# Performance work log

Measured on AMD Instinct MI355X. Metric: run time of the kernel, lower is better.

Reference implementation:

```python
import jax, jax.numpy as jnp
import numpy as np

R = 8192            # reservoir_size
CORE = int(R * 0.6)          # 4915
SHELL = int(R * 0.3)         # 2457
FB = R - CORE - SHELL        # 820
H = 1024            # lstm_hidden
IN = 1              # input_size
OUT = 1             # output_size
LEAK = 0.1
SPECTRAL = 0.9
SPARSITY = 0.3


def _scaled(key, n):
    # uniform(-1,1) NxN; spectral radius of such a matrix ~ sqrt(n * var) = sqrt(n/3).
    # Scale to ~SPECTRAL (mimics the SVD-based scaling at init without the O(n^3) SVD).
    W = jax.random.uniform(key, (n, n), jnp.float32, -1.0, 1.0)
    return W * (SPECTRAL / jnp.sqrt(n / 3.0))


def setup_inputs() -> dict:
    key = jax.random.key(0)
    ks = jax.random.split(key, 20)
    u = lambda k, sh: jax.random.uniform(k, sh, jnp.float32, -1.0, 1.0)

    W_in = u(ks[0], (R, IN))
    W_core = _scaled(ks[1], CORE)
    mask_shell = (jax.random.uniform(ks[2], (SHELL, SHELL)) < SPARSITY).astype(jnp.float32)
    W_shell = _scaled(ks[3], SHELL) * mask_shell
    W_feedback = _scaled(ks[4], FB)
    W_shell_core = u(ks[5], (CORE, SHELL))
    W_feedback_core = u(ks[6], (CORE, FB))
    dopamine = jnp.float32(0.5)
    omega = jnp.ones((R,), jnp.float32) * 2.0
    gamma = jnp.ones((R,), jnp.float32) * 0.1

    # PyTorch LSTM params, gate order [i, f, g, o]
    s = 1.0 / np.sqrt(H)
    W_ih = jax.random.uniform(ks[7], (4 * H, R), jnp.float32, -s, s)
    W_hh = jax.random.uniform(ks[8], (4 * H, H), jnp.float32, -s, s)
    b_ih = jax.random.uniform(ks[9], (4 * H,), jnp.float32, -s, s)
    b_hh = jax.random.uniform(ks[10], (4 * H,), jnp.float32, -s, s)

    W_out = jax.random.uniform(ks[11], (OUT, H), jnp.float32, -s, s)
    b_out = jax.random.uniform(ks[12], (OUT,), jnp.float32, -s, s)

    x = jax.random.normal(ks[13], (IN,), jnp.float32)
    state = jax.random.normal(ks[14], (1, R), jnp.float32)
    lstm_hidden = jax.random.normal(ks[15], (1, 1, H), jnp.float32)
    lstm_cell = jax.random.normal(ks[16], (1, 1, H), jnp.float32)

    return dict(x=x, state=state, lstm_hidden=lstm_hidden, lstm_cell=lstm_cell,
                W_in=W_in, W_core=W_core, W_shell=W_shell, W_feedback=W_feedback,
                W_shell_core=W_shell_core, W_feedback_core=W_feedback_core,
                dopamine=dopamine, omega=omega, gamma=gamma,
                W_ih=W_ih, W_hh=W_hh, b_ih=b_ih, b_hh=b_hh,
                W_out=W_out, b_out=b_out)


def reference(x, state, lstm_hidden, lstm_cell,
              W_in, W_core, W_shell, W_feedback, W_shell_core, W_feedback_core,
              dopamine, omega, gamma, W_ih, W_hh, b_ih, b_hh, W_out, b_out):
    reservoir_in = W_in @ x                      # (R,)
    core = state[:, :CORE]                       # (1, CORE)
    shell = state[:, CORE:CORE + SHELL]          # (1, SHELL)
    fb = state[:, -FB:]                          # (1, FB)

    core_pred = jnp.tanh(core @ W_core.T + reservoir_in[:CORE][None, :])
    shell_pred = jnp.tanh(shell @ W_shell.T)
    fb_pred = jnp.tanh(fb @ W_feedback.T)
    core_pred = core_pred + jnp.tanh(shell_pred @ W_shell_core.T) \
                          + jnp.tanh(fb_pred @ W_feedback_core.T)

    core_new = (1.0 - LEAK) * core + LEAK * core_pred
    shell_new = (1.0 - LEAK) * shell + LEAK * shell_pred
    fb_new = (1.0 - LEAK) * fb + LEAK * fb_pred
    s = jnp.concatenate([core_new, shell_new, fb_new], axis=1)  # (1, R)

    # harmonic oscillator update + dopamine scaling
    s = s + 0.1 * (omega * s - gamma * jnp.tanh(s))
    s = dopamine * s

    # single LSTM cell step (torch gate order i, f, g, o)
    h = lstm_hidden[0]  # (1, H)
    c = lstm_cell[0]    # (1, H)
    gates = s @ W_ih.T + b_ih + h @ W_hh.T + b_hh   # (1, 4H)
    i, f, g, o = jnp.split(gates, 4, axis=1)
    c_new = jax.nn.sigmoid(f) * c + jax.nn.sigmoid(i) * jnp.tanh(g)
    h_new = jax.nn.sigmoid(o) * jnp.tanh(c_new)

    output = h_new @ W_out.T + b_out             # (1, OUT)
    return output, s, h_new[None], c_new[None]
```

## Files before the change

kernel.cpp:

```cpp
#include <hip/hip_runtime.h>
#include <math.h>

#define R_TOT 8192
#define CORE  4915
#define SHELL 2457
#define FB    820
#define H     1024

__device__ __align__(16) float g_pred1[R_TOT];
__device__ __align__(16) float g_s[R_TOT];
__device__ __align__(16) float g_gates[4 * H];

__device__ __forceinline__ int swz(int i) { return i + (i >> 5); }
#define SWZ_SIZE(n) ((n) + (((n) - 1) >> 5))

__device__ __forceinline__ float waveReduce(float v) {
  #pragma unroll
  for (int off = 32; off; off >>= 1) v += __shfl_down(v, off, 64);
  return v;
}

__device__ __forceinline__ float sigm(float x) { return 1.f / (1.f + expf(-x)); }
__device__ __forceinline__ float dot4(float4 a, float4 b) {
  return a.x * b.x + a.y * b.y + a.z * b.z + a.w * b.w;
}

__device__ __forceinline__ float dotRowSw(const float* __restrict__ w,
                                          const float* __restrict__ xs,
                                          int xb, int N, int lane) {
  uintptr_t a = (uintptr_t)w;
  int head = (int)(((16 - (a & 15)) & 15) >> 2);
  if (head > N) head = N;
  float s0 = 0.f, s1 = 0.f, s2 = 0.f, s3 = 0.f,
        s4 = 0.f, s5 = 0.f, s6 = 0.f, s7 = 0.f;
  if (lane < head) s0 += w[lane] * xs[swz(xb + lane)];
  int nC = (N - head) >> 2;
  const float4* wv = (const float4*)(w + head);
  int b0 = xb + head;
  int c = lane;
  for (; c + 448 < nC; c += 512) {
    float4 v0 = wv[c],       v1 = wv[c + 64],  v2 = wv[c + 128], v3 = wv[c + 192],
           v4 = wv[c + 256], v5 = wv[c + 320], v6 = wv[c + 384], v7 = wv[c + 448];
    int i0 = b0 + (c << 2);
    s0 += v0.x*xs[swz(i0     )] + v0.y*xs[swz(i0+   1)] + v0.z*xs[swz(i0+   2)] + v0.w*xs[swz(i0+   3)];
    s1 += v1.x*xs[swz(i0+ 256)] + v1.y*xs[swz(i0+ 257)] + v1.z*xs[swz(i0+ 258)] + v1.w*xs[swz(i0+ 259)];
    s2 += v2.x*xs[swz(i0+ 512)] + v2.y*xs[swz(i0+ 513)] + v2.z*xs[swz(i0+ 514)] + v2.w*xs[swz(i0+ 515)];
    s3 += v3.x*xs[swz(i0+ 768)] + v3.y*xs[swz(i0+ 769)] + v3.z*xs[swz(i0+ 770)] + v3.w*xs[swz(i0+ 771)];
    s4 += v4.x*xs[swz(i0+1024)] + v4.y*xs[swz(i0+1025)] + v4.z*xs[swz(i0+1026)] + v4.w*xs[swz(i0+1027)];
    s5 += v5.x*xs[swz(i0+1280)] + v5.y*xs[swz(i0+1281)] + v5.z*xs[swz(i0+1282)] + v5.w*xs[swz(i0+1283)];
    s6 += v6.x*xs[swz(i0+1536)] + v6.y*xs[swz(i0+1537)] + v6.z*xs[swz(i0+1538)] + v6.w*xs[swz(i0+1539)];
    s7 += v7.x*xs[swz(i0+1792)] + v7.y*xs[swz(i0+1793)] + v7.z*xs[swz(i0+1794)] + v7.w*xs[swz(i0+1795)];
  }
  for (; c + 192 < nC; c += 256) {
    float4 v0 = wv[c], v1 = wv[c + 64], v2 = wv[c + 128], v3 = wv[c + 192];
    int i0 = b0 + (c << 2);
    s0 += v0.x*xs[swz(i0    )] + v0.y*xs[swz(i0+  1)] + v0.z*xs[swz(i0+  2)] + v0.w*xs[swz(i0+  3)];
    s1 += v1.x*xs[swz(i0+256)] + v1.y*xs[swz(i0+257)] + v1.z*xs[swz(i0+258)] + v1.w*xs[swz(i0+259)];
    s2 += v2.x*xs[swz(i0+512)] + v2.y*xs[swz(i0+513)] + v2.z*xs[swz(i0+514)] + v2.w*xs[swz(i0+515)];
    s3 += v3.x*xs[swz(i0+768)] + v3.y*xs[swz(i0+769)] + v3.z*xs[swz(i0+770)] + v3.w*xs[swz(i0+771)];
  }
  for (; c < nC; c += 64) {
    float4 v = wv[c];
    int i0 = b0 + (c << 2);
    s1 += v.x*xs[swz(i0)] + v.y*xs[swz(i0+1)] + v.z*xs[swz(i0+2)] + v.w*xs[swz(i0+3)];
  }
  for (int i = head + (nC << 2) + lane; i < N; i += 64)
    s2 += w[i] * xs[swz(xb + i)];
  return ((s0 + s1) + (s2 + s3)) + ((s4 + s5) + (s6 + s7));
}

__device__ __forceinline__ float dotRowAl(const float4* __restrict__ wv,
                                          const float4* __restrict__ xs4,
                                          int nC, int lane) {
  float s0 = 0.f, s1 = 0.f, s2 = 0.f, s3 = 0.f,
        s4 = 0.f, s5 = 0.f, s6 = 0.f, s7 = 0.f;
  int c = lane;
  for (; c + 448 < nC; c += 512) {
    float4 v0 = wv[c],       v1 = wv[c + 64],  v2 = wv[c + 128], v3 = wv[c + 192],
           v4 = wv[c + 256], v5 = wv[c + 320], v6 = wv[c + 384], v7 = wv[c + 448];
    s0 += dot4(v0, xs4[c      ]); s1 += dot4(v1, xs4[c + 64 ]);
    s2 += dot4(v2, xs4[c + 128]); s3 += dot4(v3, xs4[c + 192]);
    s4 += dot4(v4, xs4[c + 256]); s5 += dot4(v5, xs4[c + 320]);
    s6 += dot4(v6, xs4[c + 384]); s7 += dot4(v7, xs4[c + 448]);
  }
  for (; c + 192 < nC; c += 256) {
    float4 v0 = wv[c], v1 = wv[c + 64], v2 = wv[c + 128], v3 = wv[c + 192];
    s0 += dot4(v0, xs4[c      ]); s1 += dot4(v1, xs4[c + 64 ]);
    s2 += dot4(v2, xs4[c + 128]); s3 += dot4(v3, xs4[c + 192]);
  }
  for (; c < nC; c += 64) s1 += dot4(wv[c], xs4[c]);
  return ((s0 + s1) + (s2 + s3)) + ((s4 + s5) + (s6 + s7));
}

__device__ __forceinline__ void s_update(int i, float pred,
                                         const float* __restrict__ state,
                                         const float* __restrict__ omega,
                                         const float* __restrict__ gamma,
                                         float dopa, float* __restrict__ dout) {
  float old = state[i];
  float s1 = 0.9f * old + 0.1f * pred;
  float s2 = s1 + 0.1f * (omega[i] * s1 - gamma[i] * tanhf(s1));
  float s3 = dopa * s2;
  g_s[i] = s3;
  dout[1 + i] = s3;
}

#define NB1_CORE  ((CORE  + 3) / 4)
#define NB1_SHELL ((SHELL + 3) / 4)
#define NB1_WHH   (4 * H / 4)
#define NB1_FB    ((FB    + 3) / 4)
#define NB1_TOT   (NB1_CORE + NB1_SHELL + NB1_WHH + NB1_FB)

__global__ __launch_bounds__(256, 4) void k_stage1(
    const float* __restrict__ state, const float* __restrict__ Wcore,
    const float* __restrict__ Wshell, const float* __restrict__ Wfb,
    const float* __restrict__ Win, const float* __restrict__ xin,
    const float* __restrict__ Whh, const float* __restrict__ hin) {
  __shared__ __align__(16) float xs[SWZ_SIZE(CORE)];
  int b = blockIdx.x;
  int tid = threadIdx.x, wave = tid >> 6, lane = tid & 63;
  if (b < NB1_CORE) {
    for (int i = tid; i < CORE; i += 256) xs[swz(i)] = state[i];
    __syncthreads();
    int r = b * 4 + wave;
    if (r >= CORE) return;
    float sum = waveReduce(dotRowSw(Wcore + (size_t)r * CORE, xs, 0, CORE, lane));
    if (lane == 0) g_pred1[r] = tanhf(sum + Win[r] * xin[0]);
  } else if (b < NB1_CORE + NB1_SHELL) {
    for (int i = tid; i < SHELL; i += 256) xs[swz(i)] = state[CORE + i];
    __syncthreads();
    int r = (b - NB1_CORE) * 4 + wave;
    if (r >= SHELL) return;
    float sum = waveReduce(dotRowSw(Wshell + (size_t)r * SHELL, xs, 0, SHELL, lane));
    if (lane == 0) g_pred1[CORE + r] = tanhf(sum);
  } else if (b < NB1_CORE + NB1_SHELL + NB1_WHH) {
    float4* xs4 = (float4*)xs;
    const float4* h4 = (const float4*)hin;
    for (int i = tid; i < H / 4; i += 256) xs4[i] = h4[i];
    __syncthreads();
    int r = (b - NB1_CORE - NB1_SHELL) * 4 + wave;
    float sum = waveReduce(dotRowAl((const float4*)(Whh + (size_t)r * H), xs4, H / 4, lane));
    if (lane == 0) g_gates[r] = sum;
  } else {
    float4* xs4 = (float4*)xs;
    const float4* f4 = (const float4*)(state + CORE + SHELL);
    for (int i = tid; i < FB / 4; i += 256) xs4[i] = f4[i];
    __syncthreads();
    int r = (b - NB1_CORE - NB1_SHELL - NB1_WHH) * 4 + wave;
    if (r >= FB) return;
    float sum = waveReduce(dotRowAl((const float4*)(Wfb + (size_t)r * FB), xs4, FB / 4, lane));
    if (lane == 0) g_pred1[CORE + SHELL + r] = tanhf(sum);
  }
}

#define NB2_CORE ((CORE + 3) / 4)
#define NB2_EW   ((SHELL + FB + 255) / 256)

__global__ __launch_bounds__(256, 4) void k_stage2(
    const float* __restrict__ state,
    const float* __restrict__ Wsc, const float* __restrict__ Wfc,
    const float* __restrict__ omega, const float* __restrict__ gamma,
    const float* __restrict__ dopamine, float* __restrict__ dout) {
  __shared__ __align__(16) float  xsS[SWZ_SIZE(SHELL)];
  __shared__ __align__(16) float4 xsF[FB / 4];
  float dopa = dopamine[0];
  int b = blockIdx.x, tid = threadIdx.x;
  if (b < NB2_CORE) {
    for (int i = tid; i < SHELL; i += 256) xsS[swz(i)] = g_pred1[CORE + i];
    const float4* f4 = (const float4*)(g_pred1 + CORE + SHELL);
    for (int i = tid; i < FB / 4; i += 256) xsF[i] = f4[i];
    __syncthreads();
    int wave = tid >> 6, lane = tid & 63;
    int r = b * 4 + wave;
    if (r >= CORE) return;
    float d1 = waveReduce(dotRowSw(Wsc + (size_t)r * SHELL, xsS, 0, SHELL, lane));
    float d2 = waveReduce(dotRowAl((const float4*)(Wfc + (size_t)r * FB), xsF, FB / 4, lane));
    if (lane == 0) {
      float pred = g_pred1[r] + tanhf(d1) + tanhf(d2);
      s_update(r, pred, state, omega, gamma, dopa, dout);
    }
  } else {
    int i = CORE + (b - NB2_CORE) * 256 + tid;
    if (i < R_TOT) s_update(i, g_pred1[i], state, omega, gamma, dopa, dout);
  }
}

__global__ __launch_bounds__(256, 4) void k_gates(
    const float* __restrict__ Wih,
    const float* __restrict__ bih, const float* __restrict__ bhh) {
  __shared__ __align__(16) float4 xs4[R_TOT / 4];
  int tid = threadIdx.x;
  const float4* s4 = (const float4*)g_s;
  for (int i = tid; i < R_TOT / 4; i += 256) xs4[i] = s4[i];
  __syncthreads();
  int wave = tid >> 6, lane = tid & 63;
  int r = blockIdx.x * 4 + wave;
  float sum = waveReduce(dotRowAl((const float4*)(Wih + (size_t)r * R_TOT), xs4, R_TOT / 4, lane));
  if (lane == 0) g_gates[r] += sum + bih[r] + bhh[r];
}

__global__ __launch_bounds__(1024) void k_lstm(
    const float* __restrict__ c_in, const float* __restrict__ Wout,
    const float* __restrict__ bout, float* __restrict__ dout) {
  __shared__ float red[16];
  int j = threadIdx.x;
  float ig = g_gates[j], fg = g_gates[H + j], gg = g_gates[2 * H + j], og = g_gates[3 * H + j];
  float c = c_in[j];
  float cn = sigm(fg) * c + sigm(ig) * tanhf(gg);
  float hn = sigm(og) * tanhf(cn);
  dout[1 + R_TOT + j] = hn;
  dout[1 + R_TOT + H + j] = cn;
  float w = Wout[j] * hn;
  w = waveReduce(w);
  int wave = j >> 6, lane = j & 63;
  if (lane == 0) red[wave] = w;
  __syncthreads();
  if (j == 0) {
    float t = 0.f;
    #pragma unroll
    for (int k = 0; k < 16; ++k) t += red[k];
    dout[0] = t + bout[0];
  }
}

extern "C" void kernel_launch(void* const* d_in, const int* in_sizes, int n_in,
                              void* d_out, int out_size, void* d_ws, size_t ws_size,
                              hipStream_t stream) {
  const float *x = 0, *state = 0, *h = 0, *c = 0, *Win = 0, *Wcore = 0, *Wshell = 0,
              *Wfb = 0, *Wsc = 0, *Wfc = 0, *dopa = 0, *omega = 0, *gamma = 0,
              *Wih = 0, *Whh = 0, *bih = 0, *bhh = 0, *Wout = 0, *bout = 0;
  int n1 = 0, n1024 = 0, n8192 = 0, n4096 = 0;
  for (int i = 0; i < n_in; ++i) {
    const float* p = (const float*)d_in[i];
    switch (in_sizes[i]) {
      case 24157225: Wcore = p; break;
      case 6036849:  Wshell = p; break;
      case 672400:   Wfb = p; break;
      case 12076155: Wsc = p; break;
      case 4030300:  Wfc = p; break;
      case 33554432: Wih = p; break;
      case 4194304:  Whh = p; break;
      case 1:    { if (n1 == 0) x = p; else if (n1 == 1) dopa = p; else bout = p; n1++; } break;
      case 1024: { if (n1024 == 0) h = p; else if (n1024 == 1) c = p; else Wout = p; n1024++; } break;
      case 8192: { if (n8192 == 0) state = p; else if (n8192 == 1) Win = p;
                   else if (n8192 == 2) omega = p; else gamma = p; n8192++; } break;
      case 4096: { if (n4096 == 0) bih = p; else bhh = p; n4096++; } break;
      default: break;
    }
  }
  float* dout = (float*)d_out;

  k_stage1<<<NB1_TOT, 256, 0, stream>>>(state, Wcore, Wshell, Wfb, Win, x, Whh, h);
  k_stage2<<<NB2_CORE + NB2_EW, 256, 0, stream>>>(state, Wsc, Wfc, omega, gamma, dopa, dout);
  k_gates<<<(4 * H) / 4, 256, 0, stream>>>(Wih, bih, bhh);
  k_lstm<<<1, 1024, 0, stream>>>(c, Wout, bout, dout);
}
```

Baseline: 367.0 us.

## Compute two rows per wave and fold LSTM step into gates kernel

```diff
diff --git a/kernel.cpp b/kernel.cpp
--- a/kernel.cpp
+++ b/kernel.cpp
@@ -10,6 +10,7 @@
 __device__ __align__(16) float g_pred1[R_TOT];
 __device__ __align__(16) float g_s[R_TOT];
 __device__ __align__(16) float g_gates[4 * H];
+__device__ int g_done = 0;
 
 __device__ __forceinline__ int swz(int i) { return i + (i >> 5); }
 #define SWZ_SIZE(n) ((n) + (((n) - 1) >> 5))
@@ -25,35 +26,106 @@
   return a.x * b.x + a.y * b.y + a.z * b.z + a.w * b.w;
 }
 
+__device__ __forceinline__ float2 dotRow2Sw(const float* __restrict__ wA,
+                                            const float* __restrict__ wB,
+                                            const float* __restrict__ xs,
+                                            int N, int lane) {
+  uintptr_t a = (uintptr_t)wA;
+  int head = (int)(((16 - (a & 15)) & 15) >> 2);
+  if (head > N) head = N;
+  float a0 = 0.f, a1 = 0.f, a2 = 0.f, a3 = 0.f;
+  float b0 = 0.f, b1 = 0.f, b2 = 0.f, b3 = 0.f;
+  if (lane < head) {
+    float xv = xs[swz(lane)];
+    a0 += wA[lane] * xv; b0 += wB[lane] * xv;
+  }
+  int nC = (N - head) >> 2;
+  const float4* va = (const float4*)(wA + head);
+  const float4* vb = (const float4*)(wB + head);
+  int c = lane;
+  #define CH2(Ak, Bk, off, accA, accB) { int ii = i0 + (off);                 \
+      float x0_ = xs[swz(ii)],     x1_ = xs[swz(ii + 1)],                     \
+            x2_ = xs[swz(ii + 2)], x3_ = xs[swz(ii + 3)];                     \
+      accA += Ak.x * x0_ + Ak.y * x1_ + Ak.z * x2_ + Ak.w * x3_;              \
+      accB += Bk.x * x0_ + Bk.y * x1_ + Bk.z * x2_ + Bk.w * x3_; }
+  for (; c + 448 < nC; c += 512) {
+    float4 A0 = va[c],       A1 = va[c + 64],  A2 = va[c + 128], A3 = va[c + 192],
+           A4 = va[c + 256], A5 = va[c + 320], A6 = va[c + 384], A7 = va[c + 448];
+    float4 B0 = vb[c],       B1 = vb[c + 64],  B2 = vb[c + 128], B3 = vb[c + 192],
+           B4 = vb[c + 256], B5 = vb[c + 320], B6 = vb[c + 384], B7 = vb[c + 448];
+    int i0 = head + (c << 2);
+    CH2(A0, B0, 0,    a0, b0) CH2(A1, B1, 256,  a1, b1)
+    CH2(A2, B2, 512,  a2, b2) CH2(A3, B3, 768,  a3, b3)
+    CH2(A4, B4, 1024, a0, b0) CH2(A5, B5, 1280, a1, b1)
+    CH2(A6, B6, 1536, a2, b2) CH2(A7, B7, 1792, a3, b3)
+  }
+  for (; c + 192 < nC; c += 256) {
+    float4 A0 = va[c], A1 = va[c + 64], A2 = va[c + 128], A3 = va[c + 192];
+    float4 B0 = vb[c], B1 = vb[c + 64], B2 = vb[c + 128], B3 = vb[c + 192];
+    int i0 = head + (c << 2);
+    CH2(A0, B0, 0,   a0, b0) CH2(A1, B1, 256, a1, b1)
+    CH2(A2, B2, 512, a2, b2) CH2(A3, B3, 768, a3, b3)
+  }
+  for (; c < nC; c += 64) {
+    float4 A0 = va[c], B0 = vb[c];
+    int i0 = head + (c << 2);
+    CH2(A0, B0, 0, a0, b0)
+  }
+  #undef CH2
+  for (int i = head + (nC << 2) + lane; i < N; i += 64) {
+    float xv = xs[swz(i)];
+    a2 += wA[i] * xv; b2 += wB[i] * xv;
+  }
+  return make_float2((a0 + a1) + (a2 + a3), (b0 + b1) + (b2 + b3));
+}
+
+__device__ __forceinline__ float2 dotRow2Al(const float4* __restrict__ wa,
+                                            const float4* __restrict__ wb,
+                                            const float4* __restrict__ xs4,
+                                            int nC, int lane) {
+  float a0 = 0.f, a1 = 0.f, a2 = 0.f, a3 = 0.f;
+  float b0 = 0.f, b1 = 0.f, b2 = 0.f, b3 = 0.f;
+  int c = lane;
+  for (; c + 448 < nC; c += 512) {
+    float4 A0 = wa[c],       A1 = wa[c + 64],  A2 = wa[c + 128], A3 = wa[c + 192],
+           A4 = wa[c + 256], A5 = wa[c + 320], A6 = wa[c + 384], A7 = wa[c + 448];
+    float4 B0 = wb[c],       B1 = wb[c + 64],  B2 = wb[c + 128], B3 = wb[c + 192],
+           B4 = wb[c + 256], B5 = wb[c + 320], B6 = wb[c + 384], B7 = wb[c + 448];
+    float4 X0 = xs4[c],       X1 = xs4[c + 64],  X2 = xs4[c + 128], X3 = xs4[c + 192],
+           X4 = xs4[c + 256], X5 = xs4[c + 320], X6 = xs4[c + 384], X7 = xs4[c + 448];
+    a0 += dot4(A0, X0); b0 += dot4(B0, X0); a1 += dot4(A1, X1); b1 += dot4(B1, X1);
+    a2 += dot4(A2, X2); b2 += dot4(B2, X2); a3 += dot4(A3, X3); b3 += dot4(B3, X3);
+    a0 += dot4(A4, X4); b0 += dot4(B4, X4); a1 += dot4(A5, X5); b1 += dot4(B5, X5);
+    a2 += dot4(A6, X6); b2 += dot4(B6, X6); a3 += dot4(A7, X7); b3 += dot4(B7, X7);
+  }
+  for (; c + 192 < nC; c += 256) {
+    float4 A0 = wa[c], A1 = wa[c + 64], A2 = wa[c + 128], A3 = wa[c + 192];
+    float4 B0 = wb[c], B1 = wb[c + 64], B2 = wb[c + 128], B3 = wb[c + 192];
+    float4 X0 = xs4[c], X1 = xs4[c + 64], X2 = xs4[c + 128], X3 = xs4[c + 192];
+    a0 += dot4(A0, X0); b0 += dot4(B0, X0); a1 += dot4(A1, X1); b1 += dot4(B1, X1);
+    a2 += dot4(A2, X2); b2 += dot4(B2, X2); a3 += dot4(A3, X3); b3 += dot4(B3, X3);
+  }
+  for (; c < nC; c += 64) {
+    float4 A0 = wa[c], B0 = wb[c], X0 = xs4[c];
+    a0 += dot4(A0, X0); b0 += dot4(B0, X0);
+  }
+  return make_float2((a0 + a1) + (a2 + a3), (b0 + b1) + (b2 + b3));
+}
+
 __device__ __forceinline__ float dotRowSw(const float* __restrict__ w,
                                           const float* __restrict__ xs,
-                                          int xb, int N, int lane) {
+                                          int N, int lane) {
   uintptr_t a = (uintptr_t)w;
   int head = (int)(((16 - (a & 15)) & 15) >> 2);
   if (head > N) head = N;
-  float s0 = 0.f, s1 = 0.f, s2 = 0.f, s3 = 0.f,
-        s4 = 0.f, s5 = 0.f, s6 = 0.f, s7 = 0.f;
-  if (lane < head) s0 += w[lane] * xs[swz(xb + lane)];
+  float s0 = 0.f, s1 = 0.f, s2 = 0.f, s3 = 0.f;
+  if (lane < head) s0 += w[lane] * xs[swz(lane)];
   int nC = (N - head) >> 2;
   const float4* wv = (const float4*)(w + head);
-  int b0 = xb + head;
   int c = lane;
-  for (; c + 448 < nC; c += 512) {
-    float4 v0 = wv[c],       v1 = wv[c + 64],  v2 = wv[c + 128], v3 = wv[c + 192],
-           v4 = wv[c + 256], v5 = wv[c + 320], v6 = wv[c + 384], v7 = wv[c + 448];
-    int i0 = b0 + (c << 2);
-    s0 += v0.x*xs[swz(i0     )] + v0.y*xs[swz(i0+   1)] + v0.z*xs[swz(i0+   2)] + v0.w*xs[swz(i0+   3)];
-    s1 += v1.x*xs[swz(i0+ 256)] + v1.y*xs[swz(i0+ 257)] + v1.z*xs[swz(i0+ 258)] + v1.w*xs[swz(i0+ 259)];
-    s2 += v2.x*xs[swz(i0+ 512)] + v2.y*xs[swz(i0+ 513)] + v2.z*xs[swz(i0+ 514)] + v2.w*xs[swz(i0+ 515)];
-    s3 += v3.x*xs[swz(i0+ 768)] + v3.y*xs[swz(i0+ 769)] + v3.z*xs[swz(i0+ 770)] + v3.w*xs[swz(i0+ 771)];
-    s4 += v4.x*xs[swz(i0+1024)] + v4.y*xs[swz(i0+1025)] + v4.z*xs[swz(i0+1026)] + v4.w*xs[swz(i0+1027)];
-    s5 += v5.x*xs[swz(i0+1280)] + v5.y*xs[swz(i0+1281)] + v5.z*xs[swz(i0+1282)] + v5.w*xs[swz(i0+1283)];
-    s6 += v6.x*xs[swz(i0+1536)] + v6.y*xs[swz(i0+1537)] + v6.z*xs[swz(i0+1538)] + v6.w*xs[swz(i0+1539)];
-    s7 += v7.x*xs[swz(i0+1792)] + v7.y*xs[swz(i0+1793)] + v7.z*xs[swz(i0+1794)] + v7.w*xs[swz(i0+1795)];
-  }
   for (; c + 192 < nC; c += 256) {
     float4 v0 = wv[c], v1 = wv[c + 64], v2 = wv[c + 128], v3 = wv[c + 192];
-    int i0 = b0 + (c << 2);
+    int i0 = head + (c << 2);
     s0 += v0.x*xs[swz(i0    )] + v0.y*xs[swz(i0+  1)] + v0.z*xs[swz(i0+  2)] + v0.w*xs[swz(i0+  3)];
     s1 += v1.x*xs[swz(i0+256)] + v1.y*xs[swz(i0+257)] + v1.z*xs[swz(i0+258)] + v1.w*xs[swz(i0+259)];
     s2 += v2.x*xs[swz(i0+512)] + v2.y*xs[swz(i0+513)] + v2.z*xs[swz(i0+514)] + v2.w*xs[swz(i0+515)];
@@ -61,35 +133,26 @@
   }
   for (; c < nC; c += 64) {
     float4 v = wv[c];
-    int i0 = b0 + (c << 2);
+    int i0 = head + (c << 2);
     s1 += v.x*xs[swz(i0)] + v.y*xs[swz(i0+1)] + v.z*xs[swz(i0+2)] + v.w*xs[swz(i0+3)];
   }
   for (int i = head + (nC << 2) + lane; i < N; i += 64)
-    s2 += w[i] * xs[swz(xb + i)];
-  return ((s0 + s1) + (s2 + s3)) + ((s4 + s5) + (s6 + s7));
+    s2 += w[i] * xs[swz(i)];
+  return (s0 + s1) + (s2 + s3);
 }
 
 __device__ __forceinline__ float dotRowAl(const float4* __restrict__ wv,
                                           const float4* __restrict__ xs4,
                                           int nC, int lane) {
-  float s0 = 0.f, s1 = 0.f, s2 = 0.f, s3 = 0.f,
-        s4 = 0.f, s5 = 0.f, s6 = 0.f, s7 = 0.f;
+  float s0 = 0.f, s1 = 0.f, s2 = 0.f, s3 = 0.f;
   int c = lane;
-  for (; c + 448 < nC; c += 512) {
-    float4 v0 = wv[c],       v1 = wv[c + 64],  v2 = wv[c + 128], v3 = wv[c + 192],
-           v4 = wv[c + 256], v5 = wv[c + 320], v6 = wv[c + 384], v7 = wv[c + 448];
-    s0 += dot4(v0, xs4[c      ]); s1 += dot4(v1, xs4[c + 64 ]);
-    s2 += dot4(v2, xs4[c + 128]); s3 += dot4(v3, xs4[c + 192]);
-    s4 += dot4(v4, xs4[c + 256]); s5 += dot4(v5, xs4[c + 320]);
-    s6 += dot4(v6, xs4[c + 384]); s7 += dot4(v7, xs4[c + 448]);
-  }
   for (; c + 192 < nC; c += 256) {
     float4 v0 = wv[c], v1 = wv[c + 64], v2 = wv[c + 128], v3 = wv[c + 192];
-    s0 += dot4(v0, xs4[c      ]); s1 += dot4(v1, xs4[c + 64 ]);
+    s0 += dot4(v0, xs4[c]);       s1 += dot4(v1, xs4[c + 64]);
     s2 += dot4(v2, xs4[c + 128]); s3 += dot4(v3, xs4[c + 192]);
   }
-  for (; c < nC; c += 64) s1 += dot4(wv[c], xs4[c]);
-  return ((s0 + s1) + (s2 + s3)) + ((s4 + s5) + (s6 + s7));
+  for (; c < nC; c += 64) s0 += dot4(wv[c], xs4[c]);
+  return (s0 + s1) + (s2 + s3);
 }
 
 __device__ __forceinline__ void s_update(int i, float pred,
@@ -105,11 +168,11 @@
   dout[1 + i] = s3;
 }
 
-#define NB1_CORE  ((CORE  + 3) / 4)
-#define NB1_SHELL ((SHELL + 3) / 4)
-#define NB1_WHH   (4 * H / 4)
-#define NB1_FB    ((FB    + 3) / 4)
-#define NB1_TOT   (NB1_CORE + NB1_SHELL + NB1_WHH + NB1_FB)
+#define NB1_CORE8  ((CORE + 7) / 8)
+#define NB1_SHELL8 ((SHELL + 7) / 8)
+#define NB1_WHH8   (4 * H / 8)
+#define NB1_FB8    ((FB + 7) / 8)
+#define NB1_TOT    (NB1_CORE8 + NB1_SHELL8 + NB1_WHH8 + NB1_FB8)
 
 __global__ __launch_bounds__(256, 4) void k_stage1(
     const float* __restrict__ state, const float* __restrict__ Wcore,
@@ -117,44 +180,77 @@
     const float* __restrict__ Win, const float* __restrict__ xin,
     const float* __restrict__ Whh, const float* __restrict__ hin) {
   __shared__ __align__(16) float xs[SWZ_SIZE(CORE)];
-  int b = blockIdx.x;
-  int tid = threadIdx.x, wave = tid >> 6, lane = tid & 63;
-  if (b < NB1_CORE) {
+  int b = blockIdx.x, tid = threadIdx.x, wave = tid >> 6, lane = tid & 63;
+  if (b < NB1_CORE8) {
     for (int i = tid; i < CORE; i += 256) xs[swz(i)] = state[i];
     __syncthreads();
-    int r = b * 4 + wave;
-    if (r >= CORE) return;
-    float sum = waveReduce(dotRowSw(Wcore + (size_t)r * CORE, xs, 0, CORE, lane));
-    if (lane == 0) g_pred1[r] = tanhf(sum + Win[r] * xin[0]);
-  } else if (b < NB1_CORE + NB1_SHELL) {
+    int rA = b * 8 + wave, rB = rA + 4;
+    if (rA >= CORE) return;
+    float x0 = xin[0];
+    if (rB < CORE) {
+      float2 d = dotRow2Sw(Wcore + (size_t)rA * CORE, Wcore + (size_t)rB * CORE,
+                           xs, CORE, lane);
+      d.x = waveReduce(d.x); d.y = waveReduce(d.y);
+      if (lane == 0) {
+        g_pred1[rA] = tanhf(d.x + Win[rA] * x0);
+        g_pred1[rB] = tanhf(d.y + Win[rB] * x0);
+      }
+    } else {
+      float s = waveReduce(dotRowSw(Wcore + (size_t)rA * CORE, xs, CORE, lane));
+      if (lane == 0) g_pred1[rA] = tanhf(s + Win[rA] * x0);
+    }
+  } else if (b < NB1_CORE8 + NB1_SHELL8) {
     for (int i = tid; i < SHELL; i += 256) xs[swz(i)] = state[CORE + i];
     __syncthreads();
-    int r = (b - NB1_CORE) * 4 + wave;
-    if (r >= SHELL) return;
-    float sum = waveReduce(dotRowSw(Wshell + (size_t)r * SHELL, xs, 0, SHELL, lane));
-    if (lane == 0) g_pred1[CORE + r] = tanhf(sum);
-  } else if (b < NB1_CORE + NB1_SHELL + NB1_WHH) {
+    int rA = (b - NB1_CORE8) * 8 + wave, rB = rA + 4;
+    if (rA >= SHELL) return;
+    if (rB < SHELL) {
+      float2 d = dotRow2Sw(Wshell + (size_t)rA * SHELL, Wshell + (size_t)rB * SHELL,
+                           xs, SHELL, lane);
+      d.x = waveReduce(d.x); d.y = waveReduce(d.y);
+      if (lane == 0) {
+        g_pred1[CORE + rA] = tanhf(d.x);
+        g_pred1[CORE + rB] = tanhf(d.y);
+      }
+    } else {
+      float s = waveReduce(dotRowSw(Wshell + (size_t)rA * SHELL, xs, SHELL, lane));
+      if (lane == 0) g_pred1[CORE + rA] = tanhf(s);
+    }
+  } else if (b < NB1_CORE8 + NB1_SHELL8 + NB1_WHH8) {
     float4* xs4 = (float4*)xs;
     const float4* h4 = (const float4*)hin;
     for (int i = tid; i < H / 4; i += 256) xs4[i] = h4[i];
     __syncthreads();
-    int r = (b - NB1_CORE - NB1_SHELL) * 4 + wave;
-    float sum = waveReduce(dotRowAl((const float4*)(Whh + (size_t)r * H), xs4, H / 4, lane));
-    if (lane == 0) g_gates[r] = sum;
+    int rA = (b - NB1_CORE8 - NB1_SHELL8) * 8 + wave, rB = rA + 4;
+    float2 d = dotRow2Al((const float4*)(Whh + (size_t)rA * H),
+                         (const float4*)(Whh + (size_t)rB * H), xs4, H / 4, lane);
+    d.x = waveReduce(d.x); d.y = waveReduce(d.y);
+    if (lane == 0) { g_gates[rA] = d.x; g_gates[rB] = d.y; }
   } else {
     float4* xs4 = (float4*)xs;
     const float4* f4 = (const float4*)(state + CORE + SHELL);
     for (int i = tid; i < FB / 4; i += 256) xs4[i] = f4[i];
     __syncthreads();
-    int r = (b - NB1_CORE - NB1_SHELL - NB1_WHH) * 4 + wave;
-    if (r >= FB) return;
-    float sum = waveReduce(dotRowAl((const float4*)(Wfb + (size_t)r * FB), xs4, FB / 4, lane));
-    if (lane == 0) g_pred1[CORE + SHELL + r] = tanhf(sum);
-  }
-}
-
-#define NB2_CORE ((CORE + 3) / 4)
-#define NB2_EW   ((SHELL + FB + 255) / 256)
+    int rA = (b - NB1_CORE8 - NB1_SHELL8 - NB1_WHH8) * 8 + wave, rB = rA + 4;
+    if (rA >= FB) return;
+    if (rB < FB) {
+      float2 d = dotRow2Al((const float4*)(Wfb + (size_t)rA * FB),
+                           (const float4*)(Wfb + (size_t)rB * FB), xs4, FB / 4, lane);
+      d.x = waveReduce(d.x); d.y = waveReduce(d.y);
+      if (lane == 0) {
+        g_pred1[CORE + SHELL + rA] = tanhf(d.x);
+        g_pred1[CORE + SHELL + rB] = tanhf(d.y);
+      }
+    } else {
+      float s = waveReduce(dotRowAl((const float4*)(Wfb + (size_t)rA * FB),
+                                    xs4, FB / 4, lane));
+      if (lane == 0) g_pred1[CORE + SHELL + rA] = tanhf(s);
+    }
+  }
+}
+
+#define NB2_CORE8 ((CORE + 7) / 8)
+#define NB2_EW    ((SHELL + FB + 255) / 256)
 
 __global__ __launch_bounds__(256, 4) void k_stage2(
     const float* __restrict__ state,
@@ -165,62 +261,86 @@
   __shared__ __align__(16) float4 xsF[FB / 4];
   float dopa = dopamine[0];
   int b = blockIdx.x, tid = threadIdx.x;
-  if (b < NB2_CORE) {
+  if (b < NB2_CORE8) {
     for (int i = tid; i < SHELL; i += 256) xsS[swz(i)] = g_pred1[CORE + i];
     const float4* f4 = (const float4*)(g_pred1 + CORE + SHELL);
     for (int i = tid; i < FB / 4; i += 256) xsF[i] = f4[i];
     __syncthreads();
     int wave = tid >> 6, lane = tid & 63;
-    int r = b * 4 + wave;
-    if (r >= CORE) return;
-    float d1 = waveReduce(dotRowSw(Wsc + (size_t)r * SHELL, xsS, 0, SHELL, lane));
-    float d2 = waveReduce(dotRowAl((const float4*)(Wfc + (size_t)r * FB), xsF, FB / 4, lane));
-    if (lane == 0) {
-      float pred = g_pred1[r] + tanhf(d1) + tanhf(d2);
-      s_update(r, pred, state, omega, gamma, dopa, dout);
+    int rA = b * 8 + wave, rB = rA + 4;
+    if (rA >= CORE) return;
+    if (rB < CORE) {
+      float2 d1 = dotRow2Sw(Wsc + (size_t)rA * SHELL, Wsc + (size_t)rB * SHELL,
+                            xsS, SHELL, lane);
+      float2 d2 = dotRow2Al((const float4*)(Wfc + (size_t)rA * FB),
+                            (const float4*)(Wfc + (size_t)rB * FB), xsF, FB / 4, lane);
+      d1.x = waveReduce(d1.x); d1.y = waveReduce(d1.y);
+      d2.x = waveReduce(d2.x); d2.y = waveReduce(d2.y);
+      if (lane == 0) {
+        s_update(rA, g_pred1[rA] + tanhf(d1.x) + tanhf(d2.x), state, omega, gamma, dopa, dout);
+        s_update(rB, g_pred1[rB] + tanhf(d1.y) + tanhf(d2.y), state, omega, gamma, dopa, dout);
+      }
+    } else {
+      float d1 = waveReduce(dotRowSw(Wsc + (size_t)rA * SHELL, xsS, SHELL, lane));
+      float d2 = waveReduce(dotRowAl((const float4*)(Wfc + (size_t)rA * FB),
+                                     xsF, FB / 4, lane));
+      if (lane == 0)
+        s_update(rA, g_pred1[rA] + tanhf(d1) + tanhf(d2), state, omega, gamma, dopa, dout);
     }
   } else {
-    int i = CORE + (b - NB2_CORE) * 256 + tid;
+    int i = CORE + (b - NB2_CORE8) * 256 + tid;
     if (i < R_TOT) s_update(i, g_pred1[i], state, omega, gamma, dopa, dout);
   }
 }
+
+#define NBG (4 * H / 8)
 
 __global__ __launch_bounds__(256, 4) void k_gates(
     const float* __restrict__ Wih,
-    const float* __restrict__ bih, const float* __restrict__ bhh) {
+    const float* __restrict__ bih, const float* __restrict__ bhh,
+    const float* __restrict__ cin, const float* __restrict__ Wout,
+    const float* __restrict__ bout, float* __restrict__ dout) {
   __shared__ __align__(16) float4 xs4[R_TOT / 4];
-  int tid = threadIdx.x;
+  __shared__ float red[4];
+  __shared__ int s_last;
+  int tid = threadIdx.x, wave = tid >> 6, lane = tid & 63;
   const float4* s4 = (const float4*)g_s;
   for (int i = tid; i < R_TOT / 4; i += 256) xs4[i] = s4[i];
   __syncthreads();
-  int wave = tid >> 6, lane = tid & 63;
-  int r = blockIdx.x * 4 + wave;
-  float sum = waveReduce(dotRowAl((const float4*)(Wih + (size_t)r * R_TOT), xs4, R_TOT / 4, lane));
-  if (lane == 0) g_gates[r] += sum + bih[r] + bhh[r];
-}
-
-__global__ __launch_bounds__(1024) void k_lstm(
-    const float* __restrict__ c_in, const float* __restrict__ Wout,
-    const float* __restrict__ bout, float* __restrict__ dout) {
-  __shared__ float red[16];
-  int j = threadIdx.x;
-  float ig = g_gates[j], fg = g_gates[H + j], gg = g_gates[2 * H + j], og = g_gates[3 * H + j];
-  float c = c_in[j];
-  float cn = sigm(fg) * c + sigm(ig) * tanhf(gg);
-  float hn = sigm(og) * tanhf(cn);
-  dout[1 + R_TOT + j] = hn;
-  dout[1 + R_TOT + H + j] = cn;
-  float w = Wout[j] * hn;
-  w = waveReduce(w);
-  int wave = j >> 6, lane = j & 63;
-  if (lane == 0) red[wave] = w;
+  int rA = blockIdx.x * 8 + wave, rB = rA + 4;
+  float2 d = dotRow2Al((const float4*)(Wih + (size_t)rA * R_TOT),
+                       (const float4*)(Wih + (size_t)rB * R_TOT),
+                       xs4, R_TOT / 4, lane);
+  d.x = waveReduce(d.x); d.y = waveReduce(d.y);
+  if (lane == 0) {
+    g_gates[rA] += d.x + bih[rA] + bhh[rA];
+    g_gates[rB] += d.y + bih[rB] + bhh[rB];
+  }
+  __threadfence();
   __syncthreads();
-  if (j == 0) {
-    float t = 0.f;
-    #pragma unroll
-    for (int k = 0; k < 16; ++k) t += red[k];
-    dout[0] = t + bout[0];
-  }
+  if (tid == 0) {
+    int prev = atomicAdd(&g_done, 1);
+    s_last = (prev == (int)gridDim.x - 1);
+    if (s_last) atomicExch(&g_done, 0);
+  }
+  __syncthreads();
+  if (!s_last) return;
+  __threadfence();
+  float acc = 0.f;
+  for (int j = tid; j < H; j += 256) {
+    float ig = g_gates[j], fg = g_gates[H + j];
+    float gg = g_gates[2 * H + j], og = g_gates[3 * H + j];
+    float cc = cin[j];
+    float cn = sigm(fg) * cc + sigm(ig) * tanhf(gg);
+    float hn = sigm(og) * tanhf(cn);
+    dout[1 + R_TOT + j] = hn;
+    dout[1 + R_TOT + H + j] = cn;
+    acc += Wout[j] * hn;
+  }
+  acc = waveReduce(acc);
+  if (lane == 0) red[wave] = acc;
+  __syncthreads();
+  if (tid == 0) dout[0] = red[0] + red[1] + red[2] + red[3] + bout[0];
 }
 
 extern "C" void kernel_launch(void* const* d_in, const int* in_sizes, int n_in,
@@ -251,7 +371,6 @@
   float* dout = (float*)d_out;
 
   k_stage1<<<NB1_TOT, 256, 0, stream>>>(state, Wcore, Wshell, Wfb, Win, x, Whh, h);
-  k_stage2<<<NB2_CORE + NB2_EW, 256, 0, stream>>>(state, Wsc, Wfc, omega, gamma, dopa, dout);
-  k_gates<<<(4 * H) / 4, 256, 0, stream>>>(Wih, bih, bhh);
-  k_lstm<<<1, 1024, 0, stream>>>(c, Wout, bout, dout);
-}
+  k_stage2<<<NB2_CORE8 + NB2_EW, 256, 0, stream>>>(state, Wsc, Wfc, omega, gamma, dopa, dout);
+  k_gates<<<NBG, 256, 0, stream>>>(Wih, bih, bhh, c, Wout, bout, dout);
+}
```

New measurement: 428.0 us. 16.6% more time.

## Split W_ih gate GEMV across K-chunks and drop shared-memory swizzle

Applied to the files above, without the earlier changes.

```diff
diff --git a/kernel.cpp b/kernel.cpp
--- a/kernel.cpp
+++ b/kernel.cpp
@@ -10,9 +10,7 @@
 __device__ __align__(16) float g_pred1[R_TOT];
 __device__ __align__(16) float g_s[R_TOT];
 __device__ __align__(16) float g_gates[4 * H];
-
-__device__ __forceinline__ int swz(int i) { return i + (i >> 5); }
-#define SWZ_SIZE(n) ((n) + (((n) - 1) >> 5))
+__device__ __align__(16) float g_gpart[4][4 * H];
 
 __device__ __forceinline__ float waveReduce(float v) {
   #pragma unroll
@@ -27,69 +25,66 @@
 
 __device__ __forceinline__ float dotRowSw(const float* __restrict__ w,
                                           const float* __restrict__ xs,
-                                          int xb, int N, int lane) {
+                                          int N, int lane) {
   uintptr_t a = (uintptr_t)w;
   int head = (int)(((16 - (a & 15)) & 15) >> 2);
   if (head > N) head = N;
-  float s0 = 0.f, s1 = 0.f, s2 = 0.f, s3 = 0.f,
-        s4 = 0.f, s5 = 0.f, s6 = 0.f, s7 = 0.f;
-  if (lane < head) s0 += w[lane] * xs[swz(xb + lane)];
+  float s0 = 0.f, s1 = 0.f, s2 = 0.f, s3 = 0.f;
+  if (lane < head) s0 += w[lane] * xs[lane];
   int nC = (N - head) >> 2;
   const float4* wv = (const float4*)(w + head);
-  int b0 = xb + head;
   int c = lane;
   for (; c + 448 < nC; c += 512) {
     float4 v0 = wv[c],       v1 = wv[c + 64],  v2 = wv[c + 128], v3 = wv[c + 192],
            v4 = wv[c + 256], v5 = wv[c + 320], v6 = wv[c + 384], v7 = wv[c + 448];
-    int i0 = b0 + (c << 2);
-    s0 += v0.x*xs[swz(i0     )] + v0.y*xs[swz(i0+   1)] + v0.z*xs[swz(i0+   2)] + v0.w*xs[swz(i0+   3)];
-    s1 += v1.x*xs[swz(i0+ 256)] + v1.y*xs[swz(i0+ 257)] + v1.z*xs[swz(i0+ 258)] + v1.w*xs[swz(i0+ 259)];
-    s2 += v2.x*xs[swz(i0+ 512)] + v2.y*xs[swz(i0+ 513)] + v2.z*xs[swz(i0+ 514)] + v2.w*xs[swz(i0+ 515)];
-    s3 += v3.x*xs[swz(i0+ 768)] + v3.y*xs[swz(i0+ 769)] + v3.z*xs[swz(i0+ 770)] + v3.w*xs[swz(i0+ 771)];
-    s4 += v4.x*xs[swz(i0+1024)] + v4.y*xs[swz(i0+1025)] + v4.z*xs[swz(i0+1026)] + v4.w*xs[swz(i0+1027)];
-    s5 += v5.x*xs[swz(i0+1280)] + v5.y*xs[swz(i0+1281)] + v5.z*xs[swz(i0+1282)] + v5.w*xs[swz(i0+1283)];
-    s6 += v6.x*xs[swz(i0+1536)] + v6.y*xs[swz(i0+1537)] + v6.z*xs[swz(i0+1538)] + v6.w*xs[swz(i0+1539)];
-    s7 += v7.x*xs[swz(i0+1792)] + v7.y*xs[swz(i0+1793)] + v7.z*xs[swz(i0+1794)] + v7.w*xs[swz(i0+1795)];
+    int i0 = head + (c << 2);
+    s0 += v0.x*xs[i0     ] + v0.y*xs[i0+   1] + v0.z*xs[i0+   2] + v0.w*xs[i0+   3];
+    s1 += v1.x*xs[i0+ 256] + v1.y*xs[i0+ 257] + v1.z*xs[i0+ 258] + v1.w*xs[i0+ 259];
+    s2 += v2.x*xs[i0+ 512] + v2.y*xs[i0+ 513] + v2.z*xs[i0+ 514] + v2.w*xs[i0+ 515];
+    s3 += v3.x*xs[i0+ 768] + v3.y*xs[i0+ 769] + v3.z*xs[i0+ 770] + v3.w*xs[i0+ 771];
+    s0 += v4.x*xs[i0+1024] + v4.y*xs[i0+1025] + v4.z*xs[i0+1026] + v4.w*xs[i0+1027];
+    s1 += v5.x*xs[i0+1280] + v5.y*xs[i0+1281] + v5.z*xs[i0+1282] + v5.w*xs[i0+1283];
+    s2 += v6.x*xs[i0+1536] + v6.y*xs[i0+1537] + v6.z*xs[i0+1538] + v6.w*xs[i0+1539];
+    s3 += v7.x*xs[i0+1792] + v7.y*xs[i0+1793] + v7.z*xs[i0+1794] + v7.w*xs[i0+1795];
   }
   for (; c + 192 < nC; c += 256) {
     float4 v0 = wv[c], v1 = wv[c + 64], v2 = wv[c + 128], v3 = wv[c + 192];
-    int i0 = b0 + (c << 2);
-    s0 += v0.x*xs[swz(i0    )] + v0.y*xs[swz(i0+  1)] + v0.z*xs[swz(i0+  2)] + v0.w*xs[swz(i0+  3)];
-    s1 += v1.x*xs[swz(i0+256)] + v1.y*xs[swz(i0+257)] + v1.z*xs[swz(i0+258)] + v1.w*xs[swz(i0+259)];
-    s2 += v2.x*xs[swz(i0+512)] + v2.y*xs[swz(i0+513)] + v2.z*xs[swz(i0+514)] + v2.w*xs[swz(i0+515)];
-    s3 += v3.x*xs[swz(i0+768)] + v3.y*xs[swz(i0+769)] + v3.z*xs[swz(i0+770)] + v3.w*xs[swz(i0+771)];
+    int i0 = head + (c << 2);
+    s0 += v0.x*xs[i0    ] + v0.y*xs[i0+  1] + v0.z*xs[i0+  2] + v0.w*xs[i0+  3];
+    s1 += v1.x*xs[i0+256] + v1.y*xs[i0+257] + v1.z*xs[i0+258] + v1.w*xs[i0+259];
+    s2 += v2.x*xs[i0+512] + v2.y*xs[i0+513] + v2.z*xs[i0+514] + v2.w*xs[i0+515];
+    s3 += v3.x*xs[i0+768] + v3.y*xs[i0+769] + v3.z*xs[i0+770] + v3.w*xs[i0+771];
   }
   for (; c < nC; c += 64) {
     float4 v = wv[c];
-    int i0 = b0 + (c << 2);
-    s1 += v.x*xs[swz(i0)] + v.y*xs[swz(i0+1)] + v.z*xs[swz(i0+2)] + v.w*xs[swz(i0+3)];
+    int i0 = head + (c << 2);
+    s1 += v.x*xs[i0] + v.y*xs[i0+1] + v.z*xs[i0+2] + v.w*xs[i0+3];
   }
   for (int i = head + (nC << 2) + lane; i < N; i += 64)
-    s2 += w[i] * xs[swz(xb + i)];
-  return ((s0 + s1) + (s2 + s3)) + ((s4 + s5) + (s6 + s7));
+    s2 += w[i] * xs[i];
+  return (s0 + s1) + (s2 + s3);
 }
 
 __device__ __forceinline__ float dotRowAl(const float4* __restrict__ wv,
                                           const float4* __restrict__ xs4,
                                           int nC, int lane) {
-  float s0 = 0.f, s1 = 0.f, s2 = 0.f, s3 = 0.f,
-        s4 = 0.f, s5 = 0.f, s6 = 0.f, s7 = 0.f;
+  float s0 = 0.f, s1 = 0.f, s2 = 0.f, s3 = 0.f;
   int c = lane;
   for (; c + 448 < nC; c += 512) {
     float4 v0 = wv[c],       v1 = wv[c + 64],  v2 = wv[c + 128], v3 = wv[c + 192],
            v4 = wv[c + 256], v5 = wv[c + 320], v6 = wv[c + 384], v7 = wv[c + 448];
     s0 += dot4(v0, xs4[c      ]); s1 += dot4(v1, xs4[c + 64 ]);
     s2 += dot4(v2, xs4[c + 128]); s3 += dot4(v3, xs4[c + 192]);
-    s4 += dot4(v4, xs4[c + 256]); s5 += dot4(v5, xs4[c + 320]);
-    s6 += dot4(v6, xs4[c + 384]); s7 += dot4(v7, xs4[c + 448]);
+    s0 += dot4(v4, xs4[c + 256]); s1 += dot4(v5, xs4[c + 320]);
+    s2 += dot4(v6, xs4[c + 384]); s3 += dot4(v7, xs4[c + 448]);
   }
   for (; c + 192 < nC; c += 256) {
     float4 v0 = wv[c], v1 = wv[c + 64], v2 = wv[c + 128], v3 = wv[c + 192];
-    s0 += dot4(v0, xs4[c      ]); s1 += dot4(v1, xs4[c + 64 ]);
+    s0 += dot4(v0, xs4[c]);       s1 += dot4(v1, xs4[c + 64]);
     s2 += dot4(v2, xs4[c + 128]); s3 += dot4(v3, xs4[c + 192]);
   }
-  for (; c < nC; c += 64) s1 += dot4(wv[c], xs4[c]);
-  return ((s0 + s1) + (s2 + s3)) + ((s4 + s5) + (s6 + s7));
+  for (; c < nC; c += 64) s0 += dot4(wv[c], xs4[c]);
+  return (s0 + s1) + (s2 + s3);
 }
 
 __device__ __forceinline__ void s_update(int i, float pred,
@@ -111,36 +106,37 @@
 #define NB1_FB    ((FB    + 3) / 4)
 #define NB1_TOT   (NB1_CORE + NB1_SHELL + NB1_WHH + NB1_FB)
 
-__global__ __launch_bounds__(256, 4) void k_stage1(
+__global__ __launch_bounds__(256, 8) void k_stage1(
     const float* __restrict__ state, const float* __restrict__ Wcore,
     const float* __restrict__ Wshell, const float* __restrict__ Wfb,
     const float* __restrict__ Win, const float* __restrict__ xin,
-    const float* __restrict__ Whh, const float* __restrict__ hin) {
-  __shared__ __align__(16) float xs[SWZ_SIZE(CORE)];
-  int b = blockIdx.x;
-  int tid = threadIdx.x, wave = tid >> 6, lane = tid & 63;
+    const float* __restrict__ Whh, const float* __restrict__ hin,
+    const float* __restrict__ bih, const float* __restrict__ bhh) {
+  __shared__ __align__(16) float xs[CORE];
+  int b = blockIdx.x, tid = threadIdx.x, wave = tid >> 6, lane = tid & 63;
   if (b < NB1_CORE) {
-    for (int i = tid; i < CORE; i += 256) xs[swz(i)] = state[i];
+    for (int i = tid; i < CORE; i += 256) xs[i] = state[i];
     __syncthreads();
     int r = b * 4 + wave;
     if (r >= CORE) return;
-    float sum = waveReduce(dotRowSw(Wcore + (size_t)r * CORE, xs, 0, CORE, lane));
-    if (lane == 0) g_pred1[r] = tanhf(sum + Win[r] * xin[0]);
+    float s = waveReduce(dotRowSw(Wcore + (size_t)r * CORE, xs, CORE, lane));
+    if (lane == 0) g_pred1[r] = tanhf(s + Win[r] * xin[0]);
   } else if (b < NB1_CORE + NB1_SHELL) {
-    for (int i = tid; i < SHELL; i += 256) xs[swz(i)] = state[CORE + i];
+    for (int i = tid; i < SHELL; i += 256) xs[i] = state[CORE + i];
     __syncthreads();
     int r = (b - NB1_CORE) * 4 + wave;
     if (r >= SHELL) return;
-    float sum = waveReduce(dotRowSw(Wshell + (size_t)r * SHELL, xs, 0, SHELL, lane));
-    if (lane == 0) g_pred1[CORE + r] = tanhf(sum);
+    float s = waveReduce(dotRowSw(Wshell + (size_t)r * SHELL, xs, SHELL, lane));
+    if (lane == 0) g_pred1[CORE + r] = tanhf(s);
   } else if (b < NB1_CORE + NB1_SHELL + NB1_WHH) {
     float4* xs4 = (float4*)xs;
     const float4* h4 = (const float4*)hin;
     for (int i = tid; i < H / 4; i += 256) xs4[i] = h4[i];
     __syncthreads();
     int r = (b - NB1_CORE - NB1_SHELL) * 4 + wave;
-    float sum = waveReduce(dotRowAl((const float4*)(Whh + (size_t)r * H), xs4, H / 4, lane));
-    if (lane == 0) g_gates[r] = sum;
+    float s = waveReduce(dotRowAl((const float4*)(Whh + (size_t)r * H),
+                                  xs4, H / 4, lane));
+    if (lane == 0) g_gates[r] = s + bih[r] + bhh[r];
   } else {
     float4* xs4 = (float4*)xs;
     const float4* f4 = (const float4*)(state + CORE + SHELL);
@@ -148,33 +144,35 @@
     __syncthreads();
     int r = (b - NB1_CORE - NB1_SHELL - NB1_WHH) * 4 + wave;
     if (r >= FB) return;
-    float sum = waveReduce(dotRowAl((const float4*)(Wfb + (size_t)r * FB), xs4, FB / 4, lane));
-    if (lane == 0) g_pred1[CORE + SHELL + r] = tanhf(sum);
+    float s = waveReduce(dotRowAl((const float4*)(Wfb + (size_t)r * FB),
+                                  xs4, FB / 4, lane));
+    if (lane == 0) g_pred1[CORE + SHELL + r] = tanhf(s);
   }
 }
 
 #define NB2_CORE ((CORE + 3) / 4)
 #define NB2_EW   ((SHELL + FB + 255) / 256)
 
-__global__ __launch_bounds__(256, 4) void k_stage2(
+__global__ __launch_bounds__(256, 8) void k_stage2(
     const float* __restrict__ state,
     const float* __restrict__ Wsc, const float* __restrict__ Wfc,
     const float* __restrict__ omega, const float* __restrict__ gamma,
     const float* __restrict__ dopamine, float* __restrict__ dout) {
-  __shared__ __align__(16) float  xsS[SWZ_SIZE(SHELL)];
+  __shared__ __align__(16) float  xsS[SHELL];
   __shared__ __align__(16) float4 xsF[FB / 4];
   float dopa = dopamine[0];
   int b = blockIdx.x, tid = threadIdx.x;
   if (b < NB2_CORE) {
-    for (int i = tid; i < SHELL; i += 256) xsS[swz(i)] = g_pred1[CORE + i];
+    for (int i = tid; i < SHELL; i += 256) xsS[i] = g_pred1[CORE + i];
     const float4* f4 = (const float4*)(g_pred1 + CORE + SHELL);
     for (int i = tid; i < FB / 4; i += 256) xsF[i] = f4[i];
     __syncthreads();
     int wave = tid >> 6, lane = tid & 63;
     int r = b * 4 + wave;
     if (r >= CORE) return;
-    float d1 = waveReduce(dotRowSw(Wsc + (size_t)r * SHELL, xsS, 0, SHELL, lane));
-    float d2 = waveReduce(dotRowAl((const float4*)(Wfc + (size_t)r * FB), xsF, FB / 4, lane));
+    float d1 = waveReduce(dotRowSw(Wsc + (size_t)r * SHELL, xsS, SHELL, lane));
+    float d2 = waveReduce(dotRowAl((const float4*)(Wfc + (size_t)r * FB),
+                                   xsF, FB / 4, lane));
     if (lane == 0) {
       float pred = g_pred1[r] + tanhf(d1) + tanhf(d2);
       s_update(r, pred, state, omega, gamma, dopa, dout);
@@ -185,18 +183,29 @@
   }
 }
 
-__global__ __launch_bounds__(256, 4) void k_gates(
-    const float* __restrict__ Wih,
-    const float* __restrict__ bih, const float* __restrict__ bhh) {
-  __shared__ __align__(16) float4 xs4[R_TOT / 4];
-  int tid = threadIdx.x;
-  const float4* s4 = (const float4*)g_s;
-  for (int i = tid; i < R_TOT / 4; i += 256) xs4[i] = s4[i];
+#define GCH   4
+#define GCHN  (R_TOT / GCH)
+#define GCHV  (GCHN / 4)
+#define NBG   (4 * H / 4 * GCH)
+
+__global__ __launch_bounds__(256, 8) void k_gates(const float* __restrict__ Wih) {
+  __shared__ __align__(16) float4 xs4[GCHV];
+  int b = blockIdx.x, tid = threadIdx.x, wave = tid >> 6, lane = tid & 63;
+  int k = b & (GCH - 1);
+  int r = ((b >> 2) << 2) + wave;
+  const float4* s4 = (const float4*)g_s + k * GCHV;
+  for (int i = tid; i < GCHV; i += 256) xs4[i] = s4[i];
   __syncthreads();
-  int wave = tid >> 6, lane = tid & 63;
-  int r = blockIdx.x * 4 + wave;
-  float sum = waveReduce(dotRowAl((const float4*)(Wih + (size_t)r * R_TOT), xs4, R_TOT / 4, lane));
-  if (lane == 0) g_gates[r] += sum + bih[r] + bhh[r];
+  const float4* wv = (const float4*)(Wih + (size_t)r * R_TOT) + k * GCHV;
+  float4 A0 = wv[lane      ], A1 = wv[lane +  64], A2 = wv[lane + 128],
+         A3 = wv[lane + 192], A4 = wv[lane + 256], A5 = wv[lane + 320],
+         A6 = wv[lane + 384], A7 = wv[lane + 448];
+  float s0 = dot4(A0, xs4[lane      ]) + dot4(A1, xs4[lane +  64]);
+  float s1 = dot4(A2, xs4[lane + 128]) + dot4(A3, xs4[lane + 192]);
+  float s2 = dot4(A4, xs4[lane + 256]) + dot4(A5, xs4[lane + 320]);
+  float s3 = dot4(A6, xs4[lane + 384]) + dot4(A7, xs4[lane + 448]);
+  float d = waveReduce((s0 + s1) + (s2 + s3));
+  if (lane == 0) g_gpart[k][r] = d;
 }
 
 __global__ __launch_bounds__(1024) void k_lstm(
@@ -204,10 +213,16 @@
     const float* __restrict__ bout, float* __restrict__ dout) {
   __shared__ float red[16];
   int j = threadIdx.x;
-  float ig = g_gates[j], fg = g_gates[H + j], gg = g_gates[2 * H + j], og = g_gates[3 * H + j];
+  float gv[4];
+  #pragma unroll
+  for (int g = 0; g < 4; ++g) {
+    int idx = g * H + j;
+    gv[g] = g_gates[idx] + ((g_gpart[0][idx] + g_gpart[1][idx]) +
+                            (g_gpart[2][idx] + g_gpart[3][idx]));
+  }
   float c = c_in[j];
-  float cn = sigm(fg) * c + sigm(ig) * tanhf(gg);
-  float hn = sigm(og) * tanhf(cn);
+  float cn = sigm(gv[1]) * c + sigm(gv[0]) * tanhf(gv[2]);
+  float hn = sigm(gv[3]) * tanhf(cn);
   dout[1 + R_TOT + j] = hn;
   dout[1 + R_TOT + H + j] = cn;
   float w = Wout[j] * hn;
@@ -218,7 +233,7 @@
   if (j == 0) {
     float t = 0.f;
     #pragma unroll
-    for (int k = 0; k < 16; ++k) t += red[k];
+    for (int kk = 0; kk < 16; ++kk) t += red[kk];
     dout[0] = t + bout[0];
   }
 }
@@ -250,8 +265,10 @@
   }
   float* dout = (float*)d_out;
 
-  k_stage1<<<NB1_TOT, 256, 0, stream>>>(state, Wcore, Wshell, Wfb, Win, x, Whh, h);
-  k_stage2<<<NB2_CORE + NB2_EW, 256, 0, stream>>>(state, Wsc, Wfc, omega, gamma, dopa, dout);
-  k_gates<<<(4 * H) / 4, 256, 0, stream>>>(Wih, bih, bhh);
+  k_stage1<<<NB1_TOT, 256, 0, stream>>>(state, Wcore, Wshell, Wfb, Win, x,
+                                        Whh, h, bih, bhh);
+  k_stage2<<<NB2_CORE + NB2_EW, 256, 0, stream>>>(state, Wsc, Wfc, omega, gamma,
+                                                  dopa, dout);
+  k_gates<<<NBG, 256, 0, stream>>>(Wih);
   k_lstm<<<1, 1024, 0, stream>>>(c, Wout, bout, dout);
 }
```

Result: no change. 365.6 us (-0.4%).
